# Kernel optimization log

Measured on AMD Instinct MI355X. Metric: run time of the kernel, lower is better.

## Reference

```python
import jax, jax.numpy as jnp
import numpy as np

C = 1024
H = 16
D = C // H  # head_dim = 64
FF = 4 * C


def setup_inputs() -> dict:
    key = jax.random.key(0)
    ks = jax.random.split(key, 10)
    s = lambda fan_in: 1.0 / np.sqrt(fan_in)
    return {
        "x": jax.random.normal(ks[0], (2, 2048, C), dtype=jnp.float32),
        "ln1_g": jnp.ones((C,), jnp.float32),
        "ln1_b": jnp.zeros((C,), jnp.float32),
        "w_qkv": jax.random.normal(ks[1], (C, 3 * C), jnp.float32) * s(C),
        "w_proj": jax.random.normal(ks[2], (C, C), jnp.float32) * s(C),
        "b_proj": jnp.zeros((C,), jnp.float32),
        "ln2_g": jnp.ones((C,), jnp.float32),
        "ln2_b": jnp.zeros((C,), jnp.float32),
        "w_fc1": jax.random.normal(ks[3], (C, FF), jnp.float32) * s(C),
        "b_fc1": jnp.zeros((FF,), jnp.float32),
        "w_fc2": jax.random.normal(ks[4], (FF, C), jnp.float32) * s(FF),
        "b_fc2": jnp.zeros((C,), jnp.float32),
    }


def _layernorm(x, g, b, eps=1e-5):
    mu = jnp.mean(x, axis=-1, keepdims=True)
    var = jnp.var(x, axis=-1, keepdims=True)
    return (x - mu) * jax.lax.rsqrt(var + eps) * g + b


def reference(x, ln1_g, ln1_b, w_qkv, w_proj, b_proj, ln2_g, ln2_b, w_fc1, b_fc1, w_fc2, b_fc2):
    B, N, _ = x.shape
    scale = D ** -0.5
    # --- attention sub-block (pre-LN) ---
    h = _layernorm(x, ln1_g, ln1_b)
    qkv = (h @ w_qkv).reshape(B, N, 3, H, D)
    q, k, v = jnp.moveaxis(qkv, 2, 0)          # each [B, N, H, D]
    attn = jnp.einsum("bnhd,bmhd->bhnm", q, k) * scale  # [B,H,N,N]
    attn = jax.nn.softmax(attn, axis=-1)
    o = jnp.einsum("bhnm,bmhd->bnhd", attn, v).reshape(B, N, C)
    x = x + o @ w_proj + b_proj
    # --- MLP sub-block (pre-LN) ---
    h = _layernorm(x, ln2_g, ln2_b)
    h = jax.nn.gelu(h @ w_fc1 + b_fc1, approximate=False)
    x = x + h @ w_fc2 + b_fc2
    return x
```

## Files before the change

### kernel.cpp

```cpp
#include <hip/hip_runtime.h>
#include <hip/hip_bf16.h>

typedef unsigned short u16;
typedef unsigned int u32;
typedef __attribute__((ext_vector_type(8))) short bf16x8;
typedef __attribute__((ext_vector_type(4))) float f32x4;
typedef __attribute__((ext_vector_type(4))) int   i32x4;
typedef __attribute__((ext_vector_type(4))) float fvec4;
typedef __attribute__((ext_vector_type(4))) unsigned int u32x4;

__device__ inline u16 f2bf(float f) {
    union { float f; unsigned u; } v; v.f = f;
    unsigned r = v.u + 0x7fffu + ((v.u >> 16) & 1u);
    return (u16)(r >> 16);
}

__device__ inline u32 cvtpk(float lo, float hi) {
    u32 r;
    asm("v_cvt_pk_bf16_f32 %0, %1, %2" : "=v"(r) : "v"(lo), "v"(hi));
    return r;
}

__device__ inline f32x4 mfma16(bf16x8 a, bf16x8 b, f32x4 c) {
    return __builtin_amdgcn_mfma_f32_16x16x32_bf16(a, b, c, 0, 0, 0);
}

__device__ inline void gload16(const void* g, void* l) {
    __builtin_amdgcn_global_load_lds(
        (const __attribute__((address_space(1))) unsigned int*)g,
        (__attribute__((address_space(3))) unsigned int*)l, 16, 0, 0);
}

__global__ __launch_bounds__(256)
void transpose_all(const float* __restrict__ w0, u16* __restrict__ o0,
                   const float* __restrict__ w1, u16* __restrict__ o1,
                   const float* __restrict__ w2, u16* __restrict__ o2,
                   const float* __restrict__ w3, u16* __restrict__ o3) {
    __shared__ float tile[32][33];
    int b = blockIdx.x;
    const float* in; u16* out; int K, N, local;
    if (b < 3072)      { in = w0; out = o0; K = 1024; N = 3072; local = b; }
    else if (b < 4096) { in = w1; out = o1; K = 1024; N = 1024; local = b - 3072; }
    else if (b < 8192) { in = w2; out = o2; K = 1024; N = 4096; local = b - 4096; }
    else               { in = w3; out = o3; K = 4096; N = 1024; local = b - 8192; }
    const int nx = N >> 5;
    const int n0 = (local % nx) * 32, k0 = (local / nx) * 32;
    const int x = threadIdx.x & 31, y = threadIdx.x >> 5;
    for (int i = 0; i < 4; ++i)
        tile[y + i * 8][x] = in[(size_t)(k0 + y + i * 8) * N + n0 + x];
    __syncthreads();
    for (int i = 0; i < 4; ++i) {
        int r = y + i * 8;
        out[(size_t)(n0 + r) * K + k0 + x] = f2bf(tile[x][r]);
    }
}

__global__ __launch_bounds__(256)
void vtrans(const u16* __restrict__ qkv, u16* __restrict__ vT) {
    __shared__ u32 tl[64][33];
    const int t0 = blockIdx.x * 64, f0 = blockIdx.y * 64;
    const int a = threadIdx.x & 31, yy = threadIdx.x >> 5;
    for (int i = 0; i < 8; ++i) {
        int t = yy + i * 8;
        tl[t][a] = *(const u32*)(qkv + (size_t)(t0 + t) * 3072 + 2048 + f0 + a * 2);
    }
    __syncthreads();
    for (int i = 0; i < 8; ++i) {
        int f = yy + i * 8;
        u32 lo = tl[2 * a][f >> 1], hi = tl[2 * a + 1][f >> 1];
        u32 r = (f & 1) ? ((lo >> 16) | (hi & 0xffff0000u))
                        : ((lo & 0xffffu) | (hi << 16));
        *(u32*)(vT + (size_t)(f0 + f) * 4096 + t0 + 2 * a) = r;
    }
}

__global__ __launch_bounds__(256)
void ln_kernel(const float* __restrict__ x, const float* __restrict__ g,
               const float* __restrict__ bvec, u16* __restrict__ out) {
    __shared__ float red[2][4];
    const int row = blockIdx.x, tid = threadIdx.x;
    const float* xr = x + (size_t)row * 1024;
    fvec4 v = *(const fvec4*)(xr + tid * 4);
    float s  = v[0] + v[1] + v[2] + v[3];
    float s2 = v[0]*v[0] + v[1]*v[1] + v[2]*v[2] + v[3]*v[3];
    for (int off = 1; off < 64; off <<= 1) {
        s  += __shfl_xor(s,  off);
        s2 += __shfl_xor(s2, off);
    }
    const int w = tid >> 6;
    if ((tid & 63) == 0) { red[0][w] = s; red[1][w] = s2; }
    __syncthreads();
    s  = red[0][0] + red[0][1] + red[0][2] + red[0][3];
    s2 = red[1][0] + red[1][1] + red[1][2] + red[1][3];
    const float mu  = s * (1.0f / 1024.0f);
    const float var = s2 * (1.0f / 1024.0f) - mu * mu;
    const float rstd = rsqrtf(var + 1e-5f);
    fvec4 gv = *(const fvec4*)(g + tid * 4);
    fvec4 bv = *(const fvec4*)(bvec + tid * 4);
    u16 o4[4];
    for (int i = 0; i < 4; ++i)
        o4[i] = f2bf((v[i] - mu) * rstd * gv[i] + bv[i]);
    u32 lo = (u32)o4[0] | ((u32)o4[1] << 16);
    u32 hi = (u32)o4[2] | ((u32)o4[3] << 16);
    u32* dst = (u32*)(out + (size_t)row * 1024 + tid * 4);
    dst[0] = lo; dst[1] = hi;
}

__global__ __launch_bounds__(256)
void reduce4(const float* __restrict__ p1, const float* __restrict__ p2,
             const float* __restrict__ p3, const float* __restrict__ bias,
             const float* __restrict__ res, float* __restrict__ out) {
    const size_t base = (size_t)blockIdx.x * 1024 + threadIdx.x * 4;
    fvec4 a = *(const fvec4*)(out + base);
    fvec4 b = *(const fvec4*)(p1 + base);
    fvec4 c = *(const fvec4*)(p2 + base);
    fvec4 d = *(const fvec4*)(p3 + base);
    fvec4 r = *(const fvec4*)(res + base);
    fvec4 bi = *(const fvec4*)(bias + threadIdx.x * 4);
    fvec4 o;
#pragma unroll
    for (int i = 0; i < 4; ++i) o[i] = ((a[i] + b[i]) + (c[i] + d[i])) + bi[i] + r[i];
    *(fvec4*)(out + base) = o;
}

template <int MODE, int WM, int WN, int MT, int NT, int NYP>
__global__ __launch_bounds__(256)
void gemm64(const u16* __restrict__ A, const u16* __restrict__ Bt,
            const float* __restrict__ bias, const float* __restrict__ res,
            void* __restrict__ out, int M, int N, int K) {
    constexpr int TM = WM * MT * 16;
    constexpr int TN = WN * NT * 16;
    constexpr int AJ = TM / 64;
    constexpr int BJ = TN / 64;
    static_assert(TM == 128, "swizzle assumes 32 M-tiles");
    __shared__ __attribute__((aligned(16))) u16 sA[2 * TM * 32];
    __shared__ __attribute__((aligned(16))) u16 sB[2 * TN * 32];
    const int id = blockIdx.x;
    const int j  = id >> 3;
    const int by = (id & 7) * NYP + (j >> 5);
    const int bx = j & 31;
    const int tid = threadIdx.x;
    const int lane = tid & 63, w = tid >> 6;
    const int wm = w / WN, wn = w % WN;
    const int q = lane >> 4, l16 = lane & 15;

    f32x4 acc[MT][NT];
#pragma unroll
    for (int i = 0; i < MT; ++i)
#pragma unroll
        for (int jj = 0; jj < NT; ++jj) acc[i][jj] = (f32x4)0.0f;

    const int sr = lane >> 2;
    const int kc = (lane & 3) * 8;
    const u16* gA[AJ];
    const u16* gB[BJ];
#pragma unroll
    for (int jj = 0; jj < AJ; ++jj)
        gA[jj] = A + (size_t)(bx * TM + (jj * 4 + w) * 16 + sr) * K + kc;
#pragma unroll
    for (int jj = 0; jj < BJ; ++jj)
        gB[jj] = Bt + (size_t)(by * TN + (jj * 4 + w) * 16 + sr) * K + kc;

    for (int k0 = 0; k0 < K; k0 += 64) {
#pragma unroll
        for (int kt = 0; kt < 2; ++kt) {
#pragma unroll
            for (int jj = 0; jj < AJ; ++jj)
                gload16(gA[jj] + k0 + kt * 32, &sA[kt * TM * 32 + (jj * 4 + w) * 512]);
#pragma unroll
            for (int jj = 0; jj < BJ; ++jj)
                gload16(gB[jj] + k0 + kt * 32, &sB[kt * TN * 32 + (jj * 4 + w) * 512]);
        }
        __syncthreads();
#pragma unroll
        for (int kt = 0; kt < 2; ++kt) {
            bf16x8 af[MT], bf[NT];
#pragma unroll
            for (int mt = 0; mt < MT; ++mt)
                af[mt] = *(const bf16x8*)&sA[kt * TM * 32 +
                         (wm * MT * 16 + mt * 16 + l16) * 32 + q * 8];
#pragma unroll
            for (int nt = 0; nt < NT; ++nt)
                bf[nt] = *(const bf16x8*)&sB[kt * TN * 32 +
                         (wn * NT * 16 + nt * 16 + l16) * 32 + q * 8];
#pragma unroll
            for (int mt = 0; mt < MT; ++mt)
#pragma unroll
                for (int nt = 0; nt < NT; ++nt)
                    acc[mt][nt] = mfma16(af[mt], bf[nt], acc[mt][nt]);
        }
        __syncthreads();
    }

#pragma unroll
    for (int mt = 0; mt < MT; ++mt)
#pragma unroll
        for (int nt = 0; nt < NT; ++nt)
#pragma unroll
            for (int r = 0; r < 4; ++r) {
                const int row = bx * TM + wm * MT * 16 + mt * 16 + q * 4 + r;
                const int col = by * TN + wn * NT * 16 + nt * 16 + l16;
                const size_t idx = (size_t)row * N + col;
                float v = acc[mt][nt][r];
                if (MODE == 0) {
                    ((u16*)out)[idx] = f2bf(v);
                } else if (MODE == 1) {
                    ((float*)out)[idx] = v + bias[col] + res[idx];
                } else {
                    float t = v + bias[col];
                    ((u16*)out)[idx] = f2bf(t * 0.5f * (1.0f + erff(t * 0.70710678118f)));
                }
            }
}

template <int MODE, int SPLIT>
__global__ __launch_bounds__(512)
void gemm256(const u16* __restrict__ A, const u16* __restrict__ Bt,
             const float* __restrict__ bias, const float* __restrict__ res,
             void* __restrict__ out,
             float* __restrict__ q1, float* __restrict__ q2, float* __restrict__ q3,
             int M, int N, int K, int Kc) {
    __shared__ __attribute__((aligned(16))) u16 sA[2][16384];
    __shared__ __attribute__((aligned(16))) u16 sB[2][16384];
    const int tid  = threadIdx.x;
    const int w    = tid >> 6, lane = tid & 63;
    const int wm   = w >> 2,  wn   = w & 3;
    const int q    = lane >> 4, l16 = lane & 15;
    const int w8   = w << 3,  l8   = lane >> 3;
    const int kch  = (lane & 7) ^ l8;

    const int nwg  = gridDim.x;
    const int id   = blockIdx.x;
    const int wgid = (id & 7) * (nwg >> 3) + (id >> 3);
    int bx, by, sp;
    if (SPLIT == 1) { bx = wgid & 15; by = wgid >> 4; sp = 0; }
    else            { bx = wgid & 15; by = (wgid >> 4) & 3; sp = wgid >> 6; }

    const u16* pAs = A  + (size_t)(bx * 256 + w8 + l8) * K + kch * 8 + (size_t)sp * Kc;
    const u16* pBs = Bt + (size_t)(by * 256 + w8 + l8) * K + kch * 8 + (size_t)sp * Kc;

    const int cs0  = ((q ^ (l16 & 7)) << 4);
    const int cs1  = cs0 ^ 64;
    const int aoff = (wm * 128 + l16) * 128;
    const int boff = (wn * 64  + l16) * 128;

    f32x4 acc[8][4];
#pragma unroll
    for (int m = 0; m < 8; ++m)
#pragma unroll
        for (int n = 0; n < 4; ++n) acc[m][n] = (f32x4)0.0f;

#define GISS(P, r0, k0, SH, b_) \
    gload16((P) + (size_t)((r0) * K + (k0)), &SH[b_][((r0) + w8) * 64])

    GISS(pBs, 0, 0, sB, 0);   GISS(pBs, 64, 0, sB, 0);
    GISS(pBs, 128, 0, sB, 0); GISS(pBs, 192, 0, sB, 0);
    GISS(pAs, 0, 0, sA, 0);   GISS(pAs, 64, 0, sA, 0);
    GISS(pAs, 128, 0, sA, 0); GISS(pAs, 192, 0, sA, 0);
    GISS(pBs, 0, 64, sB, 1);  GISS(pBs, 64, 64, sB, 1);
    GISS(pBs, 128, 64, sB, 1);GISS(pBs, 192, 64, sB, 1);
    asm volatile("s_waitcnt vmcnt(4)" ::: "memory");
    __builtin_amdgcn_s_barrier();

    const int NT_ = Kc >> 6;
    for (int t = 0; t < NT_; ++t) {
        const int b  = t & 1;
        const char* bA_ = (const char*)&sA[b][0] + aoff;
        const char* bB_ = (const char*)&sB[b][0] + boff;
        const int kA = (t + 1 < NT_ ? t + 1 : t) << 6;
        const int kB = (t + 2 < NT_ ? t + 2 : t) << 6;

        if (b) { GISS(pAs, 0, kA, sA, 0); GISS(pAs, 64, kA, sA, 0);
                 GISS(pAs, 128, kA, sA, 0); GISS(pAs, 192, kA, sA, 0); }
        else   { GISS(pAs, 0, kA, sA, 1); GISS(pAs, 64, kA, sA, 1);
                 GISS(pAs, 128, kA, sA, 1); GISS(pAs, 192, kA, sA, 1); }
        bf16x8 bfr[4][2];
#pragma unroll
        for (int n = 0; n < 4; ++n) {
            bfr[n][0] = *(const bf16x8*)(bB_ + n * 2048 + cs0);
            bfr[n][1] = *(const bf16x8*)(bB_ + n * 2048 + cs1);
        }
        bf16x8 af[4][2];
#pragma unroll
        for (int m = 0; m < 4; ++m) {
            af[m][0] = *(const bf16x8*)(bA_ + m * 2048 + cs0);
            af[m][1] = *(const bf16x8*)(bA_ + m * 2048 + cs1);
        }
        __builtin_amdgcn_sched_barrier(0);
        __builtin_amdgcn_s_setprio(1);
#pragma unroll
        for (int kt = 0; kt < 2; ++kt)
#pragma unroll
            for (int m = 0; m < 4; ++m)
#pragma unroll
                for (int n = 0; n < 4; ++n)
                    acc[m][n] = mfma16(af[m][kt], bfr[n][kt], acc[m][n]);
        __builtin_amdgcn_s_setprio(0);
        __builtin_amdgcn_s_barrier();

        if (b) { GISS(pBs, 0, kB, sB, 1); GISS(pBs, 64, kB, sB, 1);
                 GISS(pBs, 128, kB, sB, 1); GISS(pBs, 192, kB, sB, 1); }
        else   { GISS(pBs, 0, kB, sB, 0); GISS(pBs, 64, kB, sB, 0);
                 GISS(pBs, 128, kB, sB, 0); GISS(pBs, 192, kB, sB, 0); }
        bf16x8 ag[4][2];
#pragma unroll
        for (int m = 0; m < 4; ++m) {
            ag[m][0] = *(const bf16x8*)(bA_ + (4 + m) * 2048 + cs0);
            ag[m][1] = *(const bf16x8*)(bA_ + (4 + m) * 2048 + cs1);
        }
        __builtin_amdgcn_sched_barrier(0);
        __builtin_amdgcn_s_setprio(1);
#pragma unroll
        for (int kt = 0; kt < 2; ++kt)
#pragma unroll
            for (int m = 0; m < 4; ++m)
#pragma unroll
                for (int n = 0; n < 4; ++n)
                    acc[4 + m][n] = mfma16(ag[m][kt], bfr[n][kt], acc[4 + m][n]);
        __builtin_amdgcn_s_setprio(0);
        asm volatile("s_waitcnt vmcnt(4)" ::: "memory");
        __builtin_amdgcn_s_barrier();
    }
#undef GISS

    float* po = nullptr;
    if (MODE == 3)
        po = sp == 0 ? (float*)out : sp == 1 ? q1 : sp == 2 ? q2 : q3;

#pragma unroll
    for (int m = 0; m < 8; ++m)
#pragma unroll
        for (int n = 0; n < 4; ++n)
#pragma unroll
            for (int r = 0; r < 4; ++r) {
                const int row = bx * 256 + wm * 128 + m * 16 + q * 4 + r;
                const int col = by * 256 + wn * 64 + n * 16 + l16;
                const size_t idx = (size_t)row * N + col;
                float v = acc[m][n][r];
                if (MODE == 0) {
                    ((u16*)out)[idx] = f2bf(v);
                } else if (MODE == 1) {
                    ((float*)out)[idx] = v + bias[col] + res[idx];
                } else if (MODE == 2) {
                    float t = v + bias[col];
                    ((u16*)out)[idx] = f2bf(t * 0.5f * (1.0f + erff(t * 0.70710678118f)));
                } else {
                    po[idx] = v;
                }
            }
}

__global__ __launch_bounds__(256)
void attention3(const u16* __restrict__ qkv, const u16* __restrict__ vT,
                u16* __restrict__ o) {
    __shared__ __attribute__((aligned(16))) u16 sK[64][72];
    __shared__ __attribute__((aligned(16))) u16 sV[64][72];

    const int tid = threadIdx.x;
    const int lane = tid & 63, w = tid >> 6;
    const int qc = lane >> 4, l16 = lane & 15;
    const int bx = blockIdx.x;
    const int qt = bx & 15, h = (bx >> 4) & 15, b = bx >> 8;
    const int rowbase = qt * 128 + w * 32;

    const float SC = 0.18033688f;

    bf16x8 aQ[2][2];
#pragma unroll
    for (int mtq = 0; mtq < 2; ++mtq)
#pragma unroll
        for (int kd = 0; kd < 2; ++kd) {
            bf16x8 qv = *(const bf16x8*)(qkv +
                (size_t)(b * 2048 + rowbase + mtq * 16 + l16) * 3072 +
                h * 64 + kd * 32 + qc * 8);
            u32x4 pw;
#pragma unroll
            for (int i = 0; i < 4; ++i) {
                union { u32 u; float f; } lo, hi;
                lo.u = (u32)(u16)(short)qv[2 * i]     << 16;
                hi.u = (u32)(u16)(short)qv[2 * i + 1] << 16;
                pw[i] = cvtpk(lo.f * SC, hi.f * SC);
            }
            aQ[mtq][kd] = *(const bf16x8*)&pw;
        }

    f32x4 accO[2][4];
#pragma unroll
    for (int mtq = 0; mtq < 2; ++mtq)
#pragma unroll
        for (int dt = 0; dt < 4; ++dt) accO[mtq][dt] = (f32x4)0.0f;
    f32x4 accS[2];
    accS[0] = (f32x4)0.0f; accS[1] = (f32x4)0.0f;

    bf16x8 vone;
#pragma unroll
    for (int i = 0; i < 8; ++i) vone[i] = (short)0x3F80;

    const int srr = tid >> 3;
    const int sc8 = (tid & 7) * 8;
    const u16* gK = qkv + (size_t)(b * 2048 + srr) * 3072 + 1024 + h * 64 + sc8;
    const u16* gV = vT + (size_t)(h * 64 + srr) * 4096 + b * 2048 + sc8;

    i32x4 cK[2], cV[2];
    cK[0] = *(const i32x4*)gK;
    cK[1] = *(const i32x4*)(gK + (size_t)32 * 3072);
    cV[0] = *(const i32x4*)gV;
    cV[1] = *(const i32x4*)(gV + (size_t)32 * 4096);

    const int sig_base = ((l16 >> 2) << 3) + (l16 & 3);

    for (int kc = 0; kc < 32; ++kc) {
        __syncthreads();
        *(i32x4*)&sK[srr][sc8]      = cK[0];
        *(i32x4*)&sK[srr + 32][sc8] = cK[1];
        *(i32x4*)&sV[srr][sc8]      = cV[0];
        *(i32x4*)&sV[srr + 32][sc8] = cV[1];
        const int kn = (kc + 1 < 32) ? kc + 1 : 31;
        i32x4 nK[2], nV[2];
        nK[0] = *(const i32x4*)(gK + (size_t)kn * 64 * 3072);
        nK[1] = *(const i32x4*)(gK + ((size_t)kn * 64 + 32) * 3072);
        nV[0] = *(const i32x4*)(gV + kn * 64);
        nV[1] = *(const i32x4*)(gV + (size_t)32 * 4096 + kn * 64);
        __syncthreads();

        bf16x8 kf[4][2];
#pragma unroll
        for (int mk = 0; mk < 4; ++mk) {
            const int krow = ((mk & 1) << 5) + ((mk >> 1) << 2) + sig_base;
            kf[mk][0] = *(const bf16x8*)&sK[krow][qc * 8];
            kf[mk][1] = *(const bf16x8*)&sK[krow][32 + qc * 8];
        }

        f32x4 s[2][4];
#pragma unroll
        for (int mtq = 0; mtq < 2; ++mtq)
#pragma unroll
            for (int mk = 0; mk < 4; ++mk) {
                f32x4 z = (f32x4)0.0f;
                z = mfma16(kf[mk][0], aQ[mtq][0], z);
                z = mfma16(kf[mk][1], aQ[mtq][1], z);
                s[mtq][mk] = z;
            }

        bf16x8 pf[2][2];
#pragma unroll
        for (int mtq = 0; mtq < 2; ++mtq) {
#pragma unroll
            for (int mk = 0; mk < 4; ++mk)
#pragma unroll
                for (int r = 0; r < 4; ++r)
                    s[mtq][mk][r] = __builtin_amdgcn_exp2f(s[mtq][mk][r]);
#pragma unroll
            for (int kt = 0; kt < 2; ++kt) {
                u32x4 pw;
                pw[0] = cvtpk(s[mtq][kt][0],     s[mtq][kt][1]);
                pw[1] = cvtpk(s[mtq][kt][2],     s[mtq][kt][3]);
                pw[2] = cvtpk(s[mtq][2 + kt][0], s[mtq][2 + kt][1]);
                pw[3] = cvtpk(s[mtq][2 + kt][2], s[mtq][2 + kt][3]);
                pf[mtq][kt] = *(const bf16x8*)&pw;
            }
        }

#pragma unroll
        for (int kt = 0; kt < 2; ++kt) {
#pragma unroll
            for (int dt = 0; dt < 4; ++dt) {
                bf16x8 vf = *(const bf16x8*)&sV[dt * 16 + l16][kt * 32 + qc * 8];
#pragma unroll
                for (int mtq = 0; mtq < 2; ++mtq)
                    accO[mtq][dt] = mfma16(pf[mtq][kt], vf, accO[mtq][dt]);
            }
#pragma unroll
            for (int mtq = 0; mtq < 2; ++mtq)
                accS[mtq] = mfma16(pf[mtq][kt], vone, accS[mtq]);
        }

        cK[0] = nK[0]; cK[1] = nK[1];
        cV[0] = nV[0]; cV[1] = nV[1];
    }

#pragma unroll
    for (int mtq = 0; mtq < 2; ++mtq)
#pragma unroll
        for (int r = 0; r < 4; ++r) {
            const float inv = 1.0f / accS[mtq][r];
            const size_t tok = (size_t)b * 2048 + rowbase + mtq * 16 + qc * 4 + r;
#pragma unroll
            for (int dt = 0; dt < 4; ++dt)
                o[tok * 1024 + h * 64 + dt * 16 + l16] = f2bf(accO[mtq][dt][r] * inv);
        }
}

extern "C" void kernel_launch(void* const* d_in, const int* in_sizes, int n_in,
                              void* d_out, int out_size, void* d_ws, size_t ws_size,
                              hipStream_t stream) {
    const float* x      = (const float*)d_in[0];
    const float* ln1_g  = (const float*)d_in[1];
    const float* ln1_b  = (const float*)d_in[2];
    const float* w_qkv  = (const float*)d_in[3];
    const float* w_proj = (const float*)d_in[4];
    const float* b_proj = (const float*)d_in[5];
    const float* ln2_g  = (const float*)d_in[6];
    const float* ln2_b  = (const float*)d_in[7];
    const float* w_fc1  = (const float*)d_in[8];
    const float* b_fc1  = (const float*)d_in[9];
    const float* w_fc2  = (const float*)d_in[10];
    const float* b_fc2  = (const float*)d_in[11];
    float* out = (float*)d_out;

    char* ws = (char*)d_ws;
    u16*   wqkvT  = (u16*)(ws + 0);
    u16*   wprojT = (u16*)(ws + 6291456);
    u16*   wfc1T  = (u16*)(ws + 8388608);
    u16*   wfc2T  = (u16*)(ws + 16777216);
    u16*   hA     = (u16*)(ws + 25165824);
    u16*   qkv    = (u16*)(ws + 33554432);
    float* x1     = (float*)(ws + 58720256);
    u16*   gbuf   = (u16*)(ws + 75497472);
    u16*   vT     = (u16*)(ws + 75497472);
    float* p1     = (float*)(ws + 0);
    float* p2     = (float*)(ws + 25165824);
    float* p3     = (float*)(ws + 41943040);

    dim3 blk(256);
    transpose_all<<<12288, blk, 0, stream>>>(w_qkv, wqkvT, w_proj, wprojT,
                                             w_fc1, wfc1T, w_fc2, wfc2T);

    ln_kernel<<<4096, blk, 0, stream>>>(x, ln1_g, ln1_b, hA);
    gemm256<0, 1><<<192, dim3(512), 0, stream>>>(hA, wqkvT, nullptr, nullptr, qkv,
                                                 nullptr, nullptr, nullptr, 4096, 3072, 1024, 1024);
    vtrans<<<dim3(64, 16), blk, 0, stream>>>(qkv, vT);
    attention3<<<512, blk, 0, stream>>>(qkv, vT, hA);
    gemm64<1, 4, 1, 2, 4, 2><<<512, blk, 0, stream>>>(hA, wprojT, b_proj, x, x1, 4096, 1024, 1024);

    u16* h2 = qkv;
    ln_kernel<<<4096, blk, 0, stream>>>(x1, ln2_g, ln2_b, h2);
    gemm256<2, 1><<<256, dim3(512), 0, stream>>>(h2, wfc1T, b_fc1, nullptr, gbuf,
                                                 nullptr, nullptr, nullptr, 4096, 4096, 1024, 1024);
    gemm256<3, 4><<<256, dim3(512), 0, stream>>>(gbuf, wfc2T, nullptr, nullptr, out,
                                                 p1, p2, p3, 4096, 1024, 4096, 1024);
    reduce4<<<4096, blk, 0, stream>>>(p1, p2, p3, b_fc2, x1, out);
}
```

Before: 358.0 us.

## Add triple-buffered 128x128 GEMM kernel for QKV and FC1 projections

Adds a new 256-thread GEMM with 128x128 output tiles, a K-step of 32, a three-stage LDS ring buffer with async global-to-LDS loads, XOR-swizzled LDS reads and an XCD-aware block remap. The QKV and FC1 GEMMs now use it instead of the 256x256 tile kernel, raising the workgroup count from 192/256 to 768/1024. The goal is better CU occupancy and load balance across the MI355X's many CUs, with load latency hidden by the deeper pipeline. The cost is less operand reuse per tile, so more total global and LDS traffic.

New measurement: 372.2 us. 1.04x slower.

```diff
diff --git a/kernel.cpp b/kernel.cpp
--- a/kernel.cpp
+++ b/kernel.cpp
@@ -350,6 +350,104 @@
             }
 }
 
+template <int MODE>
+__global__ __launch_bounds__(256)
+void gemm128b32(const u16* __restrict__ A, const u16* __restrict__ Bt,
+                const float* __restrict__ bias, const float* __restrict__ res,
+                void* __restrict__ out, int M, int N, int K) {
+    __shared__ __attribute__((aligned(16))) u16 sA[3][4096];
+    __shared__ __attribute__((aligned(16))) u16 sB[3][4096];
+    const int tid  = threadIdx.x;
+    const int w    = tid >> 6, lane = tid & 63;
+    const int wm   = w >> 1,  wn   = w & 1;
+    const int q    = lane >> 4, l16 = lane & 15;
+    const int w16  = w << 4;
+    const int srow = w16 + (lane >> 2);
+    const int csrc = (lane & 3) ^ ((lane >> 3) & 3);
+
+    const int nwg  = gridDim.x;
+    const int id   = blockIdx.x;
+    const int wgid = (id & 7) * (nwg >> 3) + (id >> 3);
+    const int bx   = wgid & 31, by = wgid >> 5;
+
+    const u16* pAs = A  + (size_t)(bx * 128 + srow) * K + csrc * 8;
+    const u16* pBs = Bt + (size_t)(by * 128 + srow) * K + csrc * 8;
+
+    const int cs   = ((q ^ ((l16 >> 1) & 3)) << 4);
+    const int aoff = (wm * 64 + l16) * 64;
+    const int boff = (wn * 64 + l16) * 64;
+
+    f32x4 acc[4][4];
+#pragma unroll
+    for (int m = 0; m < 4; ++m)
+#pragma unroll
+        for (int n = 0; n < 4; ++n) acc[m][n] = (f32x4)0.0f;
+
+#define GISS(P, r0, k0, SH, b_) \
+    gload16((P) + (size_t)((r0) * K + (k0)), &SH[b_][((r0) + w16) * 32])
+
+    GISS(pAs, 0, 0, sA, 0);  GISS(pAs, 64, 0, sA, 0);
+    GISS(pBs, 0, 0, sB, 0);  GISS(pBs, 64, 0, sB, 0);
+    GISS(pAs, 0, 32, sA, 1); GISS(pAs, 64, 32, sA, 1);
+    GISS(pBs, 0, 32, sB, 1); GISS(pBs, 64, 32, sB, 1);
+    asm volatile("s_waitcnt vmcnt(4)" ::: "memory");
+    __builtin_amdgcn_s_barrier();
+
+    const int NT_ = K >> 5;
+    int buf = 0;
+    for (int t = 0; t < NT_; ++t) {
+        const int nb = buf + 2 >= 3 ? buf - 1 : buf + 2;
+        const int kS = (t + 2 < NT_ ? t + 2 : NT_ - 1) << 5;
+
+        GISS(pAs, 0, kS, sA, nb); GISS(pAs, 64, kS, sA, nb);
+        GISS(pBs, 0, kS, sB, nb); GISS(pBs, 64, kS, sB, nb);
+
+        const char* bA_ = (const char*)&sA[buf][0] + aoff;
+        const char* bB_ = (const char*)&sB[buf][0] + boff;
+        bf16x8 af[4], bfr[4];
+#pragma unroll
+        for (int m = 0; m < 4; ++m)
+            af[m] = *(const bf16x8*)(bA_ + m * 1024 + cs);
+#pragma unroll
+        for (int n = 0; n < 4; ++n)
+            bfr[n] = *(const bf16x8*)(bB_ + n * 1024 + cs);
+
+        __builtin_amdgcn_sched_barrier(0);
+        __builtin_amdgcn_s_setprio(1);
+#pragma unroll
+        for (int m = 0; m < 4; ++m)
+#pragma unroll
+            for (int n = 0; n < 4; ++n)
+                acc[m][n] = mfma16(af[m], bfr[n], acc[m][n]);
+        __builtin_amdgcn_s_setprio(0);
+        asm volatile("s_waitcnt vmcnt(4)" ::: "memory");
+        __builtin_amdgcn_s_barrier();
+
+        buf = buf + 1 >= 3 ? 0 : buf + 1;
+    }
+#undef GISS
+
+#pragma unroll
+    for (int m = 0; m < 4; ++m)
+#pragma unroll
+        for (int n = 0; n < 4; ++n)
+#pragma unroll
+            for (int r = 0; r < 4; ++r) {
+                const int row = bx * 128 + wm * 64 + m * 16 + q * 4 + r;
+                const int col = by * 128 + wn * 64 + n * 16 + l16;
+                const size_t idx = (size_t)row * N + col;
+                float v = acc[m][n][r];
+                if (MODE == 0) {
+                    ((u16*)out)[idx] = f2bf(v);
+                } else if (MODE == 1) {
+                    ((float*)out)[idx] = v + bias[col] + res[idx];
+                } else {
+                    float t = v + bias[col];
+                    ((u16*)out)[idx] = f2bf(t * 0.5f * (1.0f + erff(t * 0.70710678118f)));
+                }
+            }
+}
+
 __global__ __launch_bounds__(256)
 void attention3(const u16* __restrict__ qkv, const u16* __restrict__ vT,
                 u16* __restrict__ o) {
@@ -527,16 +625,14 @@
                                              w_fc1, wfc1T, w_fc2, wfc2T);
 
     ln_kernel<<<4096, blk, 0, stream>>>(x, ln1_g, ln1_b, hA);
-    gemm256<0, 1><<<192, dim3(512), 0, stream>>>(hA, wqkvT, nullptr, nullptr, qkv,
-                                                 nullptr, nullptr, nullptr, 4096, 3072, 1024, 1024);
+    gemm128b32<0><<<768, blk, 0, stream>>>(hA, wqkvT, nullptr, nullptr, qkv, 4096, 3072, 1024);
     vtrans<<<dim3(64, 16), blk, 0, stream>>>(qkv, vT);
     attention3<<<512, blk, 0, stream>>>(qkv, vT, hA);
     gemm64<1, 4, 1, 2, 4, 2><<<512, blk, 0, stream>>>(hA, wprojT, b_proj, x, x1, 4096, 1024, 1024);
 
     u16* h2 = qkv;
     ln_kernel<<<4096, blk, 0, stream>>>(x1, ln2_g, ln2_b, h2);
-    gemm256<2, 1><<<256, dim3(512), 0, stream>>>(h2, wfc1T, b_fc1, nullptr, gbuf,
-                                                 nullptr, nullptr, nullptr, 4096, 4096, 1024, 1024);
+    gemm128b32<2><<<1024, blk, 0, stream>>>(h2, wfc1T, b_fc1, nullptr, gbuf, 4096, 4096, 1024);
     gemm256<3, 4><<<256, dim3(512), 0, stream>>>(gbuf, wfc2T, nullptr, nullptr, out,
                                                  p1, p2, p3, 4096, 1024, 4096, 1024);
     reduce4<<<4096, blk, 0, stream>>>(p1, p2, p3, b_fc2, x1, out);
```
